# Optimization experiments

Measured on AMD Instinct MI355X. Metric: run time of the kernel, lower is better.

The kernel has to match this reference:

```python
import jax, jax.numpy as jnp
import numpy as np

N = 16384   # nodes
E = 262144  # edges (avg degree 16)
H = 256     # hidden_dim
R = 32      # num_radial


def _lin(k, fi, fo):
    return jax.random.normal(k, (fi, fo), jnp.float32) / np.float32(np.sqrt(fi))


def setup_inputs() -> dict:
    key = jax.random.key(0)
    ks = jax.random.split(key, 16)
    h = jax.random.normal(ks[0], (N, H), jnp.float32)
    pos = jax.random.normal(ks[1], (N, 3), jnp.float32)
    edge_index = jax.random.randint(ks[2], (2, E), 0, N, dtype=jnp.int32)
    return {
        'h': h, 'pos': pos,
        # radial_basis: Linear(1,R), SiLU, Linear(R,R)
        'rb_w1': _lin(ks[3], 1, R), 'rb_b1': jnp.zeros((R,), jnp.float32),
        'rb_w2': _lin(ks[4], R, R), 'rb_b2': jnp.zeros((R,), jnp.float32),
        # edge_network: Linear(2H+R,H), SiLU, Linear(H,H), LayerNorm(H)
        'en_w1': _lin(ks[5], 2 * H + R, H), 'en_b1': jnp.zeros((H,), jnp.float32),
        'en_w2': _lin(ks[6], H, H), 'en_b2': jnp.zeros((H,), jnp.float32),
        'en_g': jnp.ones((H,), jnp.float32), 'en_bt': jnp.zeros((H,), jnp.float32),
        # node_network: Linear(2H,H), SiLU, Linear(H,H), LayerNorm(H)
        'nn_w1': _lin(ks[7], 2 * H, H), 'nn_b1': jnp.zeros((H,), jnp.float32),
        'nn_w2': _lin(ks[8], H, H), 'nn_b2': jnp.zeros((H,), jnp.float32),
        'nn_g': jnp.ones((H,), jnp.float32), 'nn_bt': jnp.zeros((H,), jnp.float32),
        # coord_network: Linear(H,H//2), SiLU, Linear(H//2,1), Tanh
        'cn_w1': _lin(ks[9], H, H // 2), 'cn_b1': jnp.zeros((H // 2,), jnp.float32),
        'cn_w2': _lin(ks[10], H // 2, 1), 'cn_b2': jnp.zeros((1,), jnp.float32),
        'edge_index': edge_index,
    }


def _ln(x, g, b, eps=1e-5):
    mu = jnp.mean(x, axis=-1, keepdims=True)
    var = jnp.var(x, axis=-1, keepdims=True)
    return (x - mu) / jnp.sqrt(var + eps) * g + b


def reference(h, pos, rb_w1, rb_b1, rb_w2, rb_b2,
              en_w1, en_b1, en_w2, en_b2, en_g, en_bt,
              nn_w1, nn_b1, nn_w2, nn_b2, nn_g, nn_bt,
              cn_w1, cn_b1, cn_w2, cn_b2, edge_index):
    row, col = edge_index[0], edge_index[1]
    rel_pos = pos[col] - pos[row]                                   # [E,3]
    # torch: norm(rel_pos + 1e-8) -> scalar eps added to the vector first
    dist = jnp.linalg.norm(rel_pos + 1e-8, axis=-1, keepdims=True)  # [E,1]
    radial = jax.nn.silu(dist @ rb_w1 + rb_b1) @ rb_w2 + rb_b2      # [E,R]
    edge_feat = jnp.concatenate([h[row], h[col], radial], axis=-1)  # [E,2H+R]
    edge_msg = _ln(jax.nn.silu(edge_feat @ en_w1 + en_b1) @ en_w2 + en_b2,
                   en_g, en_bt)                                     # [E,H]
    # PyG propagate with aggr='add': sum messages at target nodes (col)
    node_msg = jax.ops.segment_sum(edge_msg, col, num_segments=h.shape[0])
    hn_in = jnp.concatenate([h, node_msg], axis=-1)                 # [N,2H]
    h_updated = _ln(jax.nn.silu(hn_in @ nn_w1 + nn_b1) @ nn_w2 + nn_b2,
                    nn_g, nn_bt)                                    # [N,H]
    coord_w = jnp.tanh(jax.nn.silu(edge_msg @ cn_w1 + cn_b1) @ cn_w2 + cn_b2)  # [E,1]
    weighted = rel_pos * coord_w                                    # [E,3]
    pos_updates = jnp.zeros_like(pos).at[row].add(-weighted).at[col].add(weighted)
    return h_updated, pos_updates
```

## Files before the change

### kernel.cpp

```cpp
#include <hip/hip_runtime.h>
#include <hip/hip_bf16.h>


#define NN 16384
#define EE 262144
#define HH 256
#define RR 32

typedef __bf16 bf16x8 __attribute__((ext_vector_type(8)));
typedef float f32x4 __attribute__((ext_vector_type(4)));

typedef const void __attribute__((address_space(1)))* gas_ptr;
typedef void __attribute__((address_space(3)))* las_ptr;

__device__ __forceinline__ void gload16(const void* g, void* l) {
  __builtin_amdgcn_global_load_lds((gas_ptr)g, (las_ptr)l, 16, 0, 0);
}

__device__ __forceinline__ float silu_f(float x) { return x / (1.0f + __expf(-x)); }

__device__ __forceinline__ unsigned short bf_bits(float x) {
  union { __hip_bfloat16 b; unsigned short u; } v;
  v.b = __float2bfloat16(x);
  return v.u;
}
__device__ __forceinline__ float ubf(unsigned short u) {
  return __uint_as_float(((unsigned)u) << 16);
}

__global__ __launch_bounds__(256) void conv_h_kernel(const float* __restrict__ src,
                                                     __hip_bfloat16* __restrict__ dst,
                                                     int n4) {
  int i = blockIdx.x * 256 + threadIdx.x;
  if (i >= n4) return;
  float4 v = ((const float4*)src)[i];
  __hip_bfloat16* d = dst + (size_t)i * 4;
  d[0] = __float2bfloat16(v.x);
  d[1] = __float2bfloat16(v.y);
  d[2] = __float2bfloat16(v.z);
  d[3] = __float2bfloat16(v.w);
}

__global__ __launch_bounds__(256) void prep_w_kernel(
    const float* __restrict__ en_w1, const float* __restrict__ en_w2,
    const float* __restrict__ nn_w1, const float* __restrict__ nn_w2,
    const float* __restrict__ cn_w1, const float* __restrict__ rb_w2,
    const float* __restrict__ rb_b2, const float* __restrict__ en_b1,
    __hip_bfloat16* __restrict__ W2T, __hip_bfloat16* __restrict__ NW1T,
    __hip_bfloat16* __restrict__ NW2T, __hip_bfloat16* __restrict__ CW1T,
    __hip_bfloat16* __restrict__ W1abT, __hip_bfloat16* __restrict__ RWT,
    float* __restrict__ b1p) {
  int bid = blockIdx.x, tid = threadIdx.x;
  if (bid < 256) {
    int i = bid * 256 + tid, k = i >> 8, c = i & 255;
    W2T[(size_t)c * 256 + k] = __float2bfloat16(en_w2[i]);
  } else if (bid < 768) {
    int i = (bid - 256) * 256 + tid, k = i >> 8, c = i & 255;
    NW1T[(size_t)c * 512 + k] = __float2bfloat16(nn_w1[i]);
  } else if (bid < 1024) {
    int i = (bid - 768) * 256 + tid, k = i >> 8, c = i & 255;
    NW2T[(size_t)c * 256 + k] = __float2bfloat16(nn_w2[i]);
  } else if (bid < 1152) {
    int i = (bid - 1024) * 256 + tid, k = i >> 7, c = i & 127;
    CW1T[(size_t)c * 256 + k] = __float2bfloat16(cn_w1[i]);
  } else if (bid < 1408) {
    int i = (bid - 1152) * 256 + tid, k = i >> 8, c = i & 255;
    W1abT[(size_t)c * 256 + k] = __float2bfloat16(en_w1[i]);
  } else if (bid < 1664) {
    int i = (bid - 1408) * 256 + tid, k = i >> 8, c = i & 255;
    W1abT[(size_t)(256 + c) * 256 + k] = __float2bfloat16(en_w1[256 * 256 + i]);
  } else if (bid < 1696) {
    int t = (bid - 1664) * 256 + tid;
    int c = t >> 5, i = t & 31;
    float s = 0.f;
#pragma unroll
    for (int j = 0; j < 32; ++j) s += rb_w2[i * 32 + j] * en_w1[(512 + j) * 256 + c];
    RWT[c * 32 + i] = __float2bfloat16(s);
  } else {
    int c = tid;
    float s = en_b1[c];
#pragma unroll
    for (int j = 0; j < 32; ++j) s += rb_b2[j] * en_w1[(512 + j) * 256 + c];
    b1p[c] = s;
  }
}

__global__ __launch_bounds__(256) void count_kernel(const int* __restrict__ ei,
                                                    int* __restrict__ counts) {
  int e = blockIdx.x * 256 + threadIdx.x;
  if (e >= EE) return;
  atomicAdd(&counts[ei[EE + e]], 1);
}

__global__ __launch_bounds__(256) void scanA_kernel(const int* __restrict__ counts,
                                                    int* __restrict__ bsum) {
  __shared__ int ws[4];
  int t = threadIdx.x;
  int v = counts[blockIdx.x * 256 + t];
#pragma unroll
  for (int m = 1; m < 64; m <<= 1) v += __shfl_xor(v, m, 64);
  if ((t & 63) == 0) ws[t >> 6] = v;
  __syncthreads();
  if (t == 0) bsum[blockIdx.x] = ws[0] + ws[1] + ws[2] + ws[3];
}

__global__ __launch_bounds__(64) void scanB_kernel(const int* __restrict__ bsum,
                                                   int* __restrict__ bbase,
                                                   int* __restrict__ offs) {
  int t = threadIdx.x;
  int v = bsum[t], x = v;
#pragma unroll
  for (int d = 1; d < 64; d <<= 1) {
    int y = __shfl_up(x, d, 64);
    if (t >= d) x += y;
  }
  bbase[t] = x - v;
  if (t == 63) offs[NN] = x;
}

__global__ __launch_bounds__(256) void scanC_kernel(const int* __restrict__ counts,
                                                    const int* __restrict__ bbase,
                                                    int* __restrict__ offs,
                                                    int* __restrict__ cursor) {
  __shared__ int wtot[4];
  int t = threadIdx.x, wv = t >> 6, ln = t & 63;
  int base = blockIdx.x * 256;
  int v = counts[base + t], x = v;
#pragma unroll
  for (int d = 1; d < 64; d <<= 1) {
    int y = __shfl_up(x, d, 64);
    if (ln >= d) x += y;
  }
  if (ln == 63) wtot[wv] = x;
  __syncthreads();
  int add = bbase[blockIdx.x];
  for (int k = 0; k < wv; ++k) add += wtot[k];
  int excl = add + x - v;
  offs[base + t] = excl;
  cursor[base + t] = excl;
}

__global__ __launch_bounds__(256) void scatter_kernel(const int* __restrict__ ei,
                                                      int* __restrict__ cursor,
                                                      int* __restrict__ elist) {
  int e = blockIdx.x * 256 + threadIdx.x;
  if (e >= EE) return;
  int c = ei[EE + e];
  int p = atomicAdd(&cursor[c], 1);
  elist[p] = e;
}

__global__ __launch_bounds__(512) void pgemm_kernel(const __hip_bfloat16* __restrict__ A,
                                                    const __hip_bfloat16* __restrict__ BT,
                                                    __hip_bfloat16* __restrict__ out) {
  const int tid = threadIdx.x, w = tid >> 6, l = tid & 63, r = l & 15, g = l >> 4;
  const int n0 = blockIdx.x * 64;
  f32x4 acc[4][4];
#pragma unroll
  for (int a = 0; a < 4; ++a)
#pragma unroll
    for (int b = 0; b < 4; ++b) acc[a][b] = (f32x4){0.f, 0.f, 0.f, 0.f};
  for (int ks = 0; ks < 8; ++ks) {
    bf16x8 af[4], bfr[4];
#pragma unroll
    for (int fm = 0; fm < 4; ++fm)
      af[fm] = *(const bf16x8*)(A + (size_t)(n0 + fm * 16 + r) * 256 + ks * 32 + g * 8);
#pragma unroll
    for (int fn = 0; fn < 4; ++fn)
      bfr[fn] = *(const bf16x8*)(BT + (size_t)(w * 64 + fn * 16 + r) * 256 + ks * 32 + g * 8);
#pragma unroll
    for (int fm = 0; fm < 4; ++fm)
#pragma unroll
      for (int fn = 0; fn < 4; ++fn)
        acc[fm][fn] =
            __builtin_amdgcn_mfma_f32_16x16x32_bf16(af[fm], bfr[fn], acc[fm][fn], 0, 0, 0);
  }
#pragma unroll
  for (int fm = 0; fm < 4; ++fm)
#pragma unroll
    for (int fn = 0; fn < 4; ++fn) {
      int col = w * 64 + fn * 16 + r;
#pragma unroll
      for (int q = 0; q < 4; ++q) {
        int row = n0 + fm * 16 + g * 4 + q;
        out[(size_t)row * 512 + col] = __float2bfloat16(acc[fm][fn][q]);
      }
    }
}

__global__ __launch_bounds__(256, 4) void hidden_kernel(
    const __hip_bfloat16* __restrict__ Pb, const int* __restrict__ ei,
    const float* __restrict__ pos, const float* __restrict__ rb_w1,
    const float* __restrict__ rb_b1, const __hip_bfloat16* __restrict__ RWT,
    const float* __restrict__ b1p, const int* __restrict__ elist,
    __hip_bfloat16* __restrict__ hiddenb) {
  const int tid = threadIdx.x, w = tid >> 6, l = tid & 63, r = l & 15, g = l >> 4;
  const int slot = blockIdx.x * 64 + w * 16 + r;
  int e = elist[slot];
  int nr = ei[e], nc = ei[EE + e];
  float dx = pos[nc * 3 + 0] - pos[nr * 3 + 0] + 1e-8f;
  float dy = pos[nc * 3 + 1] - pos[nr * 3 + 1] + 1e-8f;
  float dz = pos[nc * 3 + 2] - pos[nr * 3 + 2] + 1e-8f;
  float d = sqrtf(dx * dx + dy * dy + dz * dz);
  bf16x8 sfrag;
#pragma unroll
  for (int j = 0; j < 8; ++j) {
    float x = d * rb_w1[g * 8 + j] + rb_b1[g * 8 + j];
    sfrag[j] = (__bf16)silu_f(x);
  }
  const unsigned short* Pu = (const unsigned short*)Pb;
  unsigned short* H = (unsigned short*)hiddenb;
  const size_t rowbase = (size_t)slot * 256;
  const int swz = (slot & 7) << 3;
#pragma unroll 4
  for (int t = 0; t < 16; ++t) {
    bf16x8 afr = *(const bf16x8*)(RWT + (size_t)(t * 16 + r) * 32 + g * 8);
    f32x4 rad = __builtin_amdgcn_mfma_f32_16x16x32_bf16(
        afr, sfrag, (f32x4){0.f, 0.f, 0.f, 0.f}, 0, 0, 0);
    int cbase = t * 16 + g * 4;
    ushort4 p1 = *(const ushort4*)(Pu + (size_t)nr * 512 + cbase);
    ushort4 p2 = *(const ushort4*)(Pu + (size_t)nc * 512 + 256 + cbase);
    float4 b1v = *(const float4*)(b1p + cbase);
    ushort4 o;
    o.x = bf_bits(silu_f(rad[0] + ubf(p1.x) + ubf(p2.x) + b1v.x));
    o.y = bf_bits(silu_f(rad[1] + ubf(p1.y) + ubf(p2.y) + b1v.y));
    o.z = bf_bits(silu_f(rad[2] + ubf(p1.z) + ubf(p2.z) + b1v.z));
    o.w = bf_bits(silu_f(rad[3] + ubf(p1.w) + ubf(p2.w) + b1v.w));
    *(ushort4*)(H + rowbase + (cbase ^ swz)) = o;
  }
}

__global__ __launch_bounds__(512, 4) void msg_kernel(
    const __hip_bfloat16* __restrict__ hiddenb, const int* __restrict__ ei,
    const float* __restrict__ pos, const __hip_bfloat16* __restrict__ W2T,
    const float* __restrict__ en_b2, const float* __restrict__ en_g,
    const float* __restrict__ en_bt, const __hip_bfloat16* __restrict__ CW1T,
    const float* __restrict__ cn_b1, const float* __restrict__ cn_w2,
    const float* __restrict__ cn_b2, const int* __restrict__ elist,
    float* __restrict__ nmsg, float* __restrict__ pos_out) {
  __shared__ __align__(16) __hip_bfloat16 A2[64 * 256];
  __shared__ float relb[64][3];
  __shared__ int srow[64], scol[64];
  __shared__ float red[8][64], redsq[8][64];
  __shared__ float mv[64][2];

  const int tid = threadIdx.x, w = tid >> 6, l = tid & 63, r = l & 15, g = l >> 4;
  const int e0 = blockIdx.x * 64;
  unsigned short* A2u = (unsigned short*)A2;

#pragma unroll
  for (int pass = 0; pass < 4; ++pass)
    gload16((const char*)hiddenb + (size_t)e0 * 512 + pass * 8192 + w * 1024 + l * 16,
            (char*)A2 + pass * 8192 + w * 1024);

  if (tid < 64) {
    int e = elist[e0 + tid];
    int r2 = ei[e], c2 = ei[EE + e];
    srow[tid] = r2;
    scol[tid] = c2;
    relb[tid][0] = pos[c2 * 3 + 0] - pos[r2 * 3 + 0];
    relb[tid][1] = pos[c2 * 3 + 1] - pos[r2 * 3 + 1];
    relb[tid][2] = pos[c2 * 3 + 2] - pos[r2 * 3 + 2];
  }
  __syncthreads();

  f32x4 acc[2][4];
#pragma unroll
  for (int a = 0; a < 2; ++a)
#pragma unroll
    for (int b = 0; b < 4; ++b) acc[a][b] = (f32x4){0.f, 0.f, 0.f, 0.f};
  for (int ks = 0; ks < 8; ++ks) {
    bf16x8 af[2], bfr[4];
#pragma unroll
    for (int mf = 0; mf < 2; ++mf)
      af[mf] = *(const bf16x8*)(W2T + (size_t)(w * 32 + mf * 16 + r) * 256 + ks * 32 + g * 8);
#pragma unroll
    for (int nf = 0; nf < 4; ++nf) {
      int row = nf * 16 + r;
      bfr[nf] = *(const bf16x8*)(A2 + row * 256 + ((ks * 32 + g * 8) ^ ((row & 7) << 3)));
    }
#pragma unroll
    for (int mf = 0; mf < 2; ++mf)
#pragma unroll
      for (int nf = 0; nf < 4; ++nf)
        acc[mf][nf] =
            __builtin_amdgcn_mfma_f32_16x16x32_bf16(af[mf], bfr[nf], acc[mf][nf], 0, 0, 0);
  }
  {
    float4 b2v0 = *(const float4*)(en_b2 + w * 32 + g * 4);
    float4 b2v1 = *(const float4*)(en_b2 + w * 32 + 16 + g * 4);
#pragma unroll
    for (int nf = 0; nf < 4; ++nf) {
      acc[0][nf][0] += b2v0.x;
      acc[0][nf][1] += b2v0.y;
      acc[0][nf][2] += b2v0.z;
      acc[0][nf][3] += b2v0.w;
      acc[1][nf][0] += b2v1.x;
      acc[1][nf][1] += b2v1.y;
      acc[1][nf][2] += b2v1.z;
      acc[1][nf][3] += b2v1.w;
    }
  }

#pragma unroll
  for (int nf = 0; nf < 4; ++nf) {
    float s = 0.f, sq = 0.f;
#pragma unroll
    for (int mf = 0; mf < 2; ++mf)
#pragma unroll
      for (int q = 0; q < 4; ++q) {
        float v = acc[mf][nf][q];
        s += v;
        sq += v * v;
      }
    s += __shfl_xor(s, 16, 64);
    s += __shfl_xor(s, 32, 64);
    sq += __shfl_xor(sq, 16, 64);
    sq += __shfl_xor(sq, 32, 64);
    if (l < 16) {
      red[w][nf * 16 + l] = s;
      redsq[w][nf * 16 + l] = sq;
    }
  }
  __syncthreads();
  if (tid < 64) {
    float s = 0.f, sq = 0.f;
#pragma unroll
    for (int k = 0; k < 8; ++k) {
      s += red[k][tid];
      sq += redsq[k][tid];
    }
    float mean = s * (1.0f / HH);
    float var = sq * (1.0f / HH) - mean * mean;
    mv[tid][0] = mean;
    mv[tid][1] = rsqrtf(var + 1e-5f);
  }
  __syncthreads();

  {
    float4 gv0 = *(const float4*)(en_g + w * 32 + g * 4);
    float4 gv1 = *(const float4*)(en_g + w * 32 + 16 + g * 4);
    float4 bv0 = *(const float4*)(en_bt + w * 32 + g * 4);
    float4 bv1 = *(const float4*)(en_bt + w * 32 + 16 + g * 4);
#pragma unroll
    for (int nf = 0; nf < 4; ++nf) {
      int e = nf * 16 + r;
      float mm = mv[e][0], rs = mv[e][1];
      int sz = (e & 7) << 3;
      ushort4 o0, o1;
      o0.x = bf_bits((acc[0][nf][0] - mm) * rs * gv0.x + bv0.x);
      o0.y = bf_bits((acc[0][nf][1] - mm) * rs * gv0.y + bv0.y);
      o0.z = bf_bits((acc[0][nf][2] - mm) * rs * gv0.z + bv0.z);
      o0.w = bf_bits((acc[0][nf][3] - mm) * rs * gv0.w + bv0.w);
      o1.x = bf_bits((acc[1][nf][0] - mm) * rs * gv1.x + bv1.x);
      o1.y = bf_bits((acc[1][nf][1] - mm) * rs * gv1.y + bv1.y);
      o1.z = bf_bits((acc[1][nf][2] - mm) * rs * gv1.z + bv1.z);
      o1.w = bf_bits((acc[1][nf][3] - mm) * rs * gv1.w + bv1.w);
      *(ushort4*)(A2u + (size_t)e * 256 + ((w * 32 + g * 4) ^ sz)) = o0;
      *(ushort4*)(A2u + (size_t)e * 256 + ((w * 32 + 16 + g * 4) ^ sz)) = o1;
    }
  }
  __syncthreads();

  f32x4 cacc[4];
#pragma unroll
  for (int a = 0; a < 4; ++a) cacc[a] = (f32x4){0.f, 0.f, 0.f, 0.f};
  for (int ks = 0; ks < 8; ++ks) {
    bf16x8 af = *(const bf16x8*)(CW1T + (size_t)(w * 16 + r) * 256 + ks * 32 + g * 8);
    bf16x8 bfr[4];
#pragma unroll
    for (int nf = 0; nf < 4; ++nf) {
      int row = nf * 16 + r;
      bfr[nf] = *(const bf16x8*)(A2 + row * 256 + ((ks * 32 + g * 8) ^ ((row & 7) << 3)));
    }
#pragma unroll
    for (int nf = 0; nf < 4; ++nf)
      cacc[nf] = __builtin_amdgcn_mfma_f32_16x16x32_bf16(af, bfr[nf], cacc[nf], 0, 0, 0);
  }
  {
    float4 cb1v = *(const float4*)(cn_b1 + w * 16 + g * 4);
    float4 cw2v = *(const float4*)(cn_w2 + w * 16 + g * 4);
#pragma unroll
    for (int nf = 0; nf < 4; ++nf) {
      float v = silu_f(cacc[nf][0] + cb1v.x) * cw2v.x +
                silu_f(cacc[nf][1] + cb1v.y) * cw2v.y +
                silu_f(cacc[nf][2] + cb1v.z) * cw2v.z +
                silu_f(cacc[nf][3] + cb1v.w) * cw2v.w;
      v += __shfl_xor(v, 16, 64);
      v += __shfl_xor(v, 32, 64);
      if (l < 16) red[w][nf * 16 + l] = v;
    }
  }

  {
    int c = tid & 255, half = tid >> 8;
    int rbeg = half * 32, rend = rbeg + 32;
    float run = 0.f;
    int cur = scol[rbeg];
    for (int row = rbeg; row < rend; ++row) {
      int nd = scol[row];
      if (nd != cur) {
        atomicAdd(&nmsg[(size_t)cur * 256 + c], run);
        run = 0.f;
        cur = nd;
      }
      run += ubf(A2u[(size_t)row * 256 + (c ^ ((row & 7) << 3))]);
    }
    atomicAdd(&nmsg[(size_t)cur * 256 + c], run);
  }
  __syncthreads();
  if (tid < 64) {
    float s = cn_b2[0];
#pragma unroll
    for (int k = 0; k < 8; ++k) s += red[k][tid];
    float wgt = tanhf(s);
    float ax = relb[tid][0], ay = relb[tid][1], az = relb[tid][2];
    int rr = srow[tid], cc = scol[tid];
    atomicAdd(&pos_out[rr * 3 + 0], -wgt * ax);
    atomicAdd(&pos_out[rr * 3 + 1], -wgt * ay);
    atomicAdd(&pos_out[rr * 3 + 2], -wgt * az);
    atomicAdd(&pos_out[cc * 3 + 0], wgt * ax);
    atomicAdd(&pos_out[cc * 3 + 1], wgt * ay);
    atomicAdd(&pos_out[cc * 3 + 2], wgt * az);
  }
}

__global__ __launch_bounds__(512, 4) void node_kernel(
    const __hip_bfloat16* __restrict__ hb, const float* __restrict__ nmsg,
    const __hip_bfloat16* __restrict__ NW1T, const float* __restrict__ nn_b1,
    const __hip_bfloat16* __restrict__ NW2T, const float* __restrict__ nn_b2,
    const float* __restrict__ nn_g, const float* __restrict__ nn_bt,
    float* __restrict__ out_h) {
  __shared__ __align__(16) __hip_bfloat16 A2[32 * 264];
  __shared__ float red[8][32], redsq[8][32];
  __shared__ float mv[32][2];
  __shared__ float gb[HH], btb[HH];
  const int tid = threadIdx.x, w = tid >> 6, l = tid & 63, r = l & 15, g = l >> 4;
  const int n0 = blockIdx.x * 32;
  if (tid < 256) {
    gb[tid] = nn_g[tid];
    btb[tid] = nn_bt[tid];
  }

  f32x4 acc[2][2];
#pragma unroll
  for (int a = 0; a < 2; ++a)
#pragma unroll
    for (int b = 0; b < 2; ++b) acc[a][b] = (f32x4){0.f, 0.f, 0.f, 0.f};
  for (int ks = 0; ks < 8; ++ks) {
    bf16x8 af[2], bfr[2];
#pragma unroll
    for (int fm = 0; fm < 2; ++fm)
      af[fm] = *(const bf16x8*)(hb + (size_t)(n0 + fm * 16 + r) * 256 + ks * 32 + g * 8);
#pragma unroll
    for (int fn = 0; fn < 2; ++fn)
      bfr[fn] = *(const bf16x8*)(NW1T + (size_t)(w * 32 + fn * 16 + r) * 512 + ks * 32 + g * 8);
#pragma unroll
    for (int fm = 0; fm < 2; ++fm)
#pragma unroll
      for (int fn = 0; fn < 2; ++fn)
        acc[fm][fn] =
            __builtin_amdgcn_mfma_f32_16x16x32_bf16(af[fm], bfr[fn], acc[fm][fn], 0, 0, 0);
  }
  for (int ks = 0; ks < 8; ++ks) {
    bf16x8 af[2], bfr[2];
#pragma unroll
    for (int fm = 0; fm < 2; ++fm) {
      const float* src = nmsg + (size_t)(n0 + fm * 16 + r) * 256 + ks * 32 + g * 8;
      float4 a0 = *(const float4*)src;
      float4 a1 = *(const float4*)(src + 4);
      bf16x8 v;
      v[0] = (__bf16)a0.x;
      v[1] = (__bf16)a0.y;
      v[2] = (__bf16)a0.z;
      v[3] = (__bf16)a0.w;
      v[4] = (__bf16)a1.x;
      v[5] = (__bf16)a1.y;
      v[6] = (__bf16)a1.z;
      v[7] = (__bf16)a1.w;
      af[fm] = v;
    }
#pragma unroll
    for (int fn = 0; fn < 2; ++fn)
      bfr[fn] =
          *(const bf16x8*)(NW1T + (size_t)(w * 32 + fn * 16 + r) * 512 + 256 + ks * 32 + g * 8);
#pragma unroll
    for (int fm = 0; fm < 2; ++fm)
#pragma unroll
      for (int fn = 0; fn < 2; ++fn)
        acc[fm][fn] =
            __builtin_amdgcn_mfma_f32_16x16x32_bf16(af[fm], bfr[fn], acc[fm][fn], 0, 0, 0);
  }
  __syncthreads();
#pragma unroll
  for (int fn = 0; fn < 2; ++fn) {
    int col = w * 32 + fn * 16 + r;
    float b1 = nn_b1[col];
#pragma unroll
    for (int fm = 0; fm < 2; ++fm)
#pragma unroll
      for (int q = 0; q < 4; ++q) {
        int row = fm * 16 + g * 4 + q;
        A2[row * 264 + col] = __float2bfloat16(silu_f(acc[fm][fn][q] + b1));
      }
  }
  __syncthreads();

#pragma unroll
  for (int a = 0; a < 2; ++a)
#pragma unroll
    for (int b = 0; b < 2; ++b) acc[a][b] = (f32x4){0.f, 0.f, 0.f, 0.f};
  for (int ks = 0; ks < 8; ++ks) {
    bf16x8 af[2], bfr[2];
#pragma unroll
    for (int fm = 0; fm < 2; ++fm)
      af[fm] = *(const bf16x8*)(A2 + (fm * 16 + r) * 264 + ks * 32 + g * 8);
#pragma unroll
    for (int fn = 0; fn < 2; ++fn)
      bfr[fn] = *(const bf16x8*)(NW2T + (size_t)(w * 32 + fn * 16 + r) * 256 + ks * 32 + g * 8);
#pragma unroll
    for (int fm = 0; fm < 2; ++fm)
#pragma unroll
      for (int fn = 0; fn < 2; ++fn)
        acc[fm][fn] =
            __builtin_amdgcn_mfma_f32_16x16x32_bf16(af[fm], bfr[fn], acc[fm][fn], 0, 0, 0);
  }
#pragma unroll
  for (int fn = 0; fn < 2; ++fn) {
    float b2 = nn_b2[w * 32 + fn * 16 + r];
#pragma unroll
    for (int fm = 0; fm < 2; ++fm)
#pragma unroll
      for (int q = 0; q < 4; ++q) acc[fm][fn][q] += b2;
  }
#pragma unroll
  for (int fm = 0; fm < 2; ++fm)
#pragma unroll
    for (int q = 0; q < 4; ++q) {
      float s = acc[fm][0][q] + acc[fm][1][q];
      float sq = acc[fm][0][q] * acc[fm][0][q] + acc[fm][1][q] * acc[fm][1][q];
#pragma unroll
      for (int m = 1; m < 16; m <<= 1) {
        s += __shfl_xor(s, m, 64);
        sq += __shfl_xor(sq, m, 64);
      }
      if (r == 0) {
        red[w][fm * 16 + g * 4 + q] = s;
        redsq[w][fm * 16 + g * 4 + q] = sq;
      }
    }
  __syncthreads();
  if (tid < 32) {
    float s = 0.f, sq = 0.f;
#pragma unroll
    for (int k = 0; k < 8; ++k) {
      s += red[k][tid];
      sq += redsq[k][tid];
    }
    float mean = s * (1.0f / HH);
    float var = sq * (1.0f / HH) - mean * mean;
    mv[tid][0] = mean;
    mv[tid][1] = rsqrtf(var + 1e-5f);
  }
  __syncthreads();
#pragma unroll
  for (int fn = 0; fn < 2; ++fn) {
    int col = w * 32 + fn * 16 + r;
    float gg = gb[col], bb = btb[col];
#pragma unroll
    for (int fm = 0; fm < 2; ++fm)
#pragma unroll
      for (int q = 0; q < 4; ++q) {
        int row = fm * 16 + g * 4 + q;
        out_h[(size_t)(n0 + row) * HH + col] =
            (acc[fm][fn][q] - mv[row][0]) * mv[row][1] * gg + bb;
      }
  }
}

extern "C" void kernel_launch(void* const* d_in, const int* in_sizes, int n_in,
                              void* d_out, int out_size, void* d_ws, size_t ws_size,
                              hipStream_t stream) {
  const float* h = (const float*)d_in[0];
  const float* pos = (const float*)d_in[1];
  const float* rb_w1 = (const float*)d_in[2];
  const float* rb_b1 = (const float*)d_in[3];
  const float* rb_w2 = (const float*)d_in[4];
  const float* rb_b2 = (const float*)d_in[5];
  const float* en_w1 = (const float*)d_in[6];
  const float* en_b1 = (const float*)d_in[7];
  const float* en_w2 = (const float*)d_in[8];
  const float* en_b2 = (const float*)d_in[9];
  const float* en_g = (const float*)d_in[10];
  const float* en_bt = (const float*)d_in[11];
  const float* nn_w1 = (const float*)d_in[12];
  const float* nn_b1 = (const float*)d_in[13];
  const float* nn_w2 = (const float*)d_in[14];
  const float* nn_b2 = (const float*)d_in[15];
  const float* nn_g = (const float*)d_in[16];
  const float* nn_bt = (const float*)d_in[17];
  const float* cn_w1 = (const float*)d_in[18];
  const float* cn_b1 = (const float*)d_in[19];
  const float* cn_w2 = (const float*)d_in[20];
  const float* cn_b2 = (const float*)d_in[21];
  const int* ei = (const int*)d_in[22];

  float* out_h = (float*)d_out;
  float* out_pos = out_h + (size_t)NN * HH;

  char* p = (char*)d_ws;
  auto alloc = [&p](size_t bytes) {
    char* q = p;
    p += (bytes + 255) & ~(size_t)255;
    return q;
  };
  __hip_bfloat16* hb = (__hip_bfloat16*)alloc((size_t)NN * HH * 2);
  __hip_bfloat16* Pb = (__hip_bfloat16*)alloc((size_t)NN * 512 * 2);
  __hip_bfloat16* W1abT = (__hip_bfloat16*)alloc((size_t)512 * 256 * 2);
  __hip_bfloat16* W2T = (__hip_bfloat16*)alloc((size_t)256 * 256 * 2);
  __hip_bfloat16* NW1T = (__hip_bfloat16*)alloc((size_t)256 * 512 * 2);
  __hip_bfloat16* NW2T = (__hip_bfloat16*)alloc((size_t)256 * 256 * 2);
  __hip_bfloat16* CW1T = (__hip_bfloat16*)alloc((size_t)128 * 256 * 2);
  __hip_bfloat16* RWT = (__hip_bfloat16*)alloc((size_t)256 * 32 * 2);
  float* b1p = (float*)alloc((size_t)256 * 4);
  __hip_bfloat16* hiddenb = (__hip_bfloat16*)alloc((size_t)EE * HH * 2);
  float* nmsg = (float*)alloc((size_t)NN * HH * 4);
  int* counts = (int*)alloc((size_t)NN * 4);
  int* offs = (int*)alloc((size_t)(NN + 1) * 4);
  int* cursor = (int*)alloc((size_t)NN * 4);
  int* elist = (int*)alloc((size_t)EE * 4);
  int* bsum = (int*)alloc((size_t)64 * 4);
  int* bbase = (int*)alloc((size_t)64 * 4);

  hipMemsetAsync(out_pos, 0, (size_t)NN * 3 * sizeof(float), stream);
  hipMemsetAsync(counts, 0, (size_t)NN * sizeof(int), stream);
  hipMemsetAsync(nmsg, 0, (size_t)NN * HH * sizeof(float), stream);

  prep_w_kernel<<<1697, 256, 0, stream>>>(en_w1, en_w2, nn_w1, nn_w2, cn_w1, rb_w2, rb_b2,
                                          en_b1, W2T, NW1T, NW2T, CW1T, W1abT, RWT, b1p);
  conv_h_kernel<<<(NN * HH / 4 + 255) / 256, 256, 0, stream>>>(h, hb, NN * HH / 4);
  count_kernel<<<EE / 256, 256, 0, stream>>>(ei, counts);
  scanA_kernel<<<NN / 256, 256, 0, stream>>>(counts, bsum);
  scanB_kernel<<<1, 64, 0, stream>>>(bsum, bbase, offs);
  scanC_kernel<<<NN / 256, 256, 0, stream>>>(counts, bbase, offs, cursor);
  scatter_kernel<<<EE / 256, 256, 0, stream>>>(ei, cursor, elist);
  pgemm_kernel<<<NN / 64, 512, 0, stream>>>(hb, W1abT, Pb);
  hidden_kernel<<<EE / 64, 256, 0, stream>>>(Pb, ei, pos, rb_w1, rb_b1, RWT, b1p, elist,
                                             hiddenb);
  msg_kernel<<<EE / 64, 512, 0, stream>>>(hiddenb, ei, pos, W2T, en_b2, en_g, en_bt, CW1T,
                                          cn_b1, cn_w2, cn_b2, elist, nmsg, out_pos);
  node_kernel<<<NN / 32, 512, 0, stream>>>(hb, nmsg, NW1T, nn_b1, NW2T, nn_b2, nn_g, nn_bt,
                                           out_h);
}
```

Baseline: 540.8 us.

## Fuse hidden and message kernels into one per-wave edge kernel

```diff
diff --git a/kernel.cpp b/kernel.cpp
--- a/kernel.cpp
+++ b/kernel.cpp
@@ -9,13 +9,6 @@
 
 typedef __bf16 bf16x8 __attribute__((ext_vector_type(8)));
 typedef float f32x4 __attribute__((ext_vector_type(4)));
-
-typedef const void __attribute__((address_space(1)))* gas_ptr;
-typedef void __attribute__((address_space(3)))* las_ptr;
-
-__device__ __forceinline__ void gload16(const void* g, void* l) {
-  __builtin_amdgcn_global_load_lds((gas_ptr)g, (las_ptr)l, 16, 0, 0);
-}
 
 __device__ __forceinline__ float silu_f(float x) { return x / (1.0f + __expf(-x)); }
 
@@ -188,30 +181,40 @@
     }
 }
 
-__global__ __launch_bounds__(256, 4) void hidden_kernel(
+#define WROW 260
+__global__ __launch_bounds__(256, 3) void edge_fused_kernel(
     const __hip_bfloat16* __restrict__ Pb, const int* __restrict__ ei,
     const float* __restrict__ pos, const float* __restrict__ rb_w1,
     const float* __restrict__ rb_b1, const __hip_bfloat16* __restrict__ RWT,
-    const float* __restrict__ b1p, const int* __restrict__ elist,
-    __hip_bfloat16* __restrict__ hiddenb) {
+    const float* __restrict__ b1p, const __hip_bfloat16* __restrict__ W2T,
+    const float* __restrict__ en_b2, const float* __restrict__ en_g,
+    const float* __restrict__ en_bt, const __hip_bfloat16* __restrict__ CW1T,
+    const float* __restrict__ cn_b1, const float* __restrict__ cn_w2,
+    const float* __restrict__ cn_b2, const int* __restrict__ elist,
+    float* __restrict__ nmsg, float* __restrict__ pos_out) {
+  __shared__ __align__(16) unsigned short ldsbuf[4][16 * WROW];
+  __shared__ int colmeta[4][16];
   const int tid = threadIdx.x, w = tid >> 6, l = tid & 63, r = l & 15, g = l >> 4;
+  unsigned short* WB = &ldsbuf[w][0];
+
   const int slot = blockIdx.x * 64 + w * 16 + r;
-  int e = elist[slot];
-  int nr = ei[e], nc = ei[EE + e];
-  float dx = pos[nc * 3 + 0] - pos[nr * 3 + 0] + 1e-8f;
-  float dy = pos[nc * 3 + 1] - pos[nr * 3 + 1] + 1e-8f;
-  float dz = pos[nc * 3 + 2] - pos[nr * 3 + 2] + 1e-8f;
-  float d = sqrtf(dx * dx + dy * dy + dz * dz);
+  const int e = elist[slot];
+  const int nr = ei[e], nc = ei[EE + e];
+  float dx = pos[nc * 3 + 0] - pos[nr * 3 + 0];
+  float dy = pos[nc * 3 + 1] - pos[nr * 3 + 1];
+  float dz = pos[nc * 3 + 2] - pos[nr * 3 + 2];
+  float ex = dx + 1e-8f, ey = dy + 1e-8f, ez = dz + 1e-8f;
+  float d = sqrtf(ex * ex + ey * ey + ez * ez);
+  if (g == 0) colmeta[w][r] = nc;
+
   bf16x8 sfrag;
 #pragma unroll
   for (int j = 0; j < 8; ++j) {
     float x = d * rb_w1[g * 8 + j] + rb_b1[g * 8 + j];
     sfrag[j] = (__bf16)silu_f(x);
   }
+
   const unsigned short* Pu = (const unsigned short*)Pb;
-  unsigned short* H = (unsigned short*)hiddenb;
-  const size_t rowbase = (size_t)slot * 256;
-  const int swz = (slot & 7) << 3;
 #pragma unroll 4
   for (int t = 0; t < 16; ++t) {
     bf16x8 afr = *(const bf16x8*)(RWT + (size_t)(t * 16 + r) * 32 + g * 8);
@@ -226,202 +229,109 @@
     o.y = bf_bits(silu_f(rad[1] + ubf(p1.y) + ubf(p2.y) + b1v.y));
     o.z = bf_bits(silu_f(rad[2] + ubf(p1.z) + ubf(p2.z) + b1v.z));
     o.w = bf_bits(silu_f(rad[3] + ubf(p1.w) + ubf(p2.w) + b1v.w));
-    *(ushort4*)(H + rowbase + (cbase ^ swz)) = o;
-  }
-}
-
-__global__ __launch_bounds__(512, 4) void msg_kernel(
-    const __hip_bfloat16* __restrict__ hiddenb, const int* __restrict__ ei,
-    const float* __restrict__ pos, const __hip_bfloat16* __restrict__ W2T,
-    const float* __restrict__ en_b2, const float* __restrict__ en_g,
-    const float* __restrict__ en_bt, const __hip_bfloat16* __restrict__ CW1T,
-    const float* __restrict__ cn_b1, const float* __restrict__ cn_w2,
-    const float* __restrict__ cn_b2, const int* __restrict__ elist,
-    float* __restrict__ nmsg, float* __restrict__ pos_out) {
-  __shared__ __align__(16) __hip_bfloat16 A2[64 * 256];
-  __shared__ float relb[64][3];
-  __shared__ int srow[64], scol[64];
-  __shared__ float red[8][64], redsq[8][64];
-  __shared__ float mv[64][2];
-
-  const int tid = threadIdx.x, w = tid >> 6, l = tid & 63, r = l & 15, g = l >> 4;
-  const int e0 = blockIdx.x * 64;
-  unsigned short* A2u = (unsigned short*)A2;
-
-#pragma unroll
-  for (int pass = 0; pass < 4; ++pass)
-    gload16((const char*)hiddenb + (size_t)e0 * 512 + pass * 8192 + w * 1024 + l * 16,
-            (char*)A2 + pass * 8192 + w * 1024);
-
-  if (tid < 64) {
-    int e = elist[e0 + tid];
-    int r2 = ei[e], c2 = ei[EE + e];
-    srow[tid] = r2;
-    scol[tid] = c2;
-    relb[tid][0] = pos[c2 * 3 + 0] - pos[r2 * 3 + 0];
-    relb[tid][1] = pos[c2 * 3 + 1] - pos[r2 * 3 + 1];
-    relb[tid][2] = pos[c2 * 3 + 2] - pos[r2 * 3 + 2];
-  }
-  __syncthreads();
-
-  f32x4 acc[2][4];
-#pragma unroll
-  for (int a = 0; a < 2; ++a)
-#pragma unroll
-    for (int b = 0; b < 4; ++b) acc[a][b] = (f32x4){0.f, 0.f, 0.f, 0.f};
+    *(ushort4*)(WB + r * WROW + cbase) = o;
+  }
+
+  f32x4 acc[16];
+#pragma unroll
+  for (int a = 0; a < 16; ++a) acc[a] = (f32x4){0.f, 0.f, 0.f, 0.f};
   for (int ks = 0; ks < 8; ++ks) {
-    bf16x8 af[2], bfr[4];
-#pragma unroll
-    for (int mf = 0; mf < 2; ++mf)
-      af[mf] = *(const bf16x8*)(W2T + (size_t)(w * 32 + mf * 16 + r) * 256 + ks * 32 + g * 8);
-#pragma unroll
-    for (int nf = 0; nf < 4; ++nf) {
-      int row = nf * 16 + r;
-      bfr[nf] = *(const bf16x8*)(A2 + row * 256 + ((ks * 32 + g * 8) ^ ((row & 7) << 3)));
-    }
-#pragma unroll
-    for (int mf = 0; mf < 2; ++mf)
-#pragma unroll
-      for (int nf = 0; nf < 4; ++nf)
-        acc[mf][nf] =
-            __builtin_amdgcn_mfma_f32_16x16x32_bf16(af[mf], bfr[nf], acc[mf][nf], 0, 0, 0);
-  }
+    bf16x8 bfr = *(const bf16x8*)(WB + r * WROW + ks * 32 + g * 8);
+#pragma unroll
+    for (int mf = 0; mf < 16; ++mf) {
+      bf16x8 af = *(const bf16x8*)(W2T + (size_t)(mf * 16 + r) * 256 + ks * 32 + g * 8);
+      acc[mf] = __builtin_amdgcn_mfma_f32_16x16x32_bf16(af, bfr, acc[mf], 0, 0, 0);
+    }
+  }
+
+  float s = 0.f, sq = 0.f;
+#pragma unroll
+  for (int mf = 0; mf < 16; ++mf) {
+    float4 b2v = *(const float4*)(en_b2 + mf * 16 + g * 4);
+#pragma unroll
+    for (int q = 0; q < 4; ++q) {
+      float v = acc[mf][q] + ((const float*)&b2v)[q];
+      acc[mf][q] = v;
+      s += v;
+      sq += v * v;
+    }
+  }
+  s += __shfl_xor(s, 16, 64);
+  s += __shfl_xor(s, 32, 64);
+  sq += __shfl_xor(sq, 16, 64);
+  sq += __shfl_xor(sq, 32, 64);
+  float mean = s * (1.0f / HH);
+  float rstd = rsqrtf(sq * (1.0f / HH) - mean * mean + 1e-5f);
+
+#pragma unroll
+  for (int mf = 0; mf < 16; ++mf) {
+    float4 gv = *(const float4*)(en_g + mf * 16 + g * 4);
+    float4 bv = *(const float4*)(en_bt + mf * 16 + g * 4);
+    ushort4 o;
+    o.x = bf_bits((acc[mf][0] - mean) * rstd * gv.x + bv.x);
+    o.y = bf_bits((acc[mf][1] - mean) * rstd * gv.y + bv.y);
+    o.z = bf_bits((acc[mf][2] - mean) * rstd * gv.z + bv.z);
+    o.w = bf_bits((acc[mf][3] - mean) * rstd * gv.w + bv.w);
+    *(ushort4*)(WB + r * WROW + mf * 16 + g * 4) = o;
+  }
+
+  f32x4 cacc[8];
+#pragma unroll
+  for (int a = 0; a < 8; ++a) cacc[a] = (f32x4){0.f, 0.f, 0.f, 0.f};
+  for (int ks = 0; ks < 8; ++ks) {
+    bf16x8 bfr = *(const bf16x8*)(WB + r * WROW + ks * 32 + g * 8);
+#pragma unroll
+    for (int mf = 0; mf < 8; ++mf) {
+      bf16x8 af = *(const bf16x8*)(CW1T + (size_t)(mf * 16 + r) * 256 + ks * 32 + g * 8);
+      cacc[mf] = __builtin_amdgcn_mfma_f32_16x16x32_bf16(af, bfr, cacc[mf], 0, 0, 0);
+    }
+  }
+  float vsum = 0.f;
+#pragma unroll
+  for (int mf = 0; mf < 8; ++mf) {
+    float4 cb = *(const float4*)(cn_b1 + mf * 16 + g * 4);
+    float4 cw = *(const float4*)(cn_w2 + mf * 16 + g * 4);
+    vsum += silu_f(cacc[mf][0] + cb.x) * cw.x;
+    vsum += silu_f(cacc[mf][1] + cb.y) * cw.y;
+    vsum += silu_f(cacc[mf][2] + cb.z) * cw.z;
+    vsum += silu_f(cacc[mf][3] + cb.w) * cw.w;
+  }
+  vsum += __shfl_xor(vsum, 16, 64);
+  vsum += __shfl_xor(vsum, 32, 64);
+  if (g == 0) {
+    float wgt = tanhf(vsum + cn_b2[0]);
+    atomicAdd(&pos_out[nr * 3 + 0], -wgt * dx);
+    atomicAdd(&pos_out[nr * 3 + 1], -wgt * dy);
+    atomicAdd(&pos_out[nr * 3 + 2], -wgt * dz);
+    atomicAdd(&pos_out[nc * 3 + 0], wgt * dx);
+    atomicAdd(&pos_out[nc * 3 + 1], wgt * dy);
+    atomicAdd(&pos_out[nc * 3 + 2], wgt * dz);
+  }
+
   {
-    float4 b2v0 = *(const float4*)(en_b2 + w * 32 + g * 4);
-    float4 b2v1 = *(const float4*)(en_b2 + w * 32 + 16 + g * 4);
-#pragma unroll
-    for (int nf = 0; nf < 4; ++nf) {
-      acc[0][nf][0] += b2v0.x;
-      acc[0][nf][1] += b2v0.y;
-      acc[0][nf][2] += b2v0.z;
-      acc[0][nf][3] += b2v0.w;
-      acc[1][nf][0] += b2v1.x;
-      acc[1][nf][1] += b2v1.y;
-      acc[1][nf][2] += b2v1.z;
-      acc[1][nf][3] += b2v1.w;
-    }
-  }
-
-#pragma unroll
-  for (int nf = 0; nf < 4; ++nf) {
-    float s = 0.f, sq = 0.f;
-#pragma unroll
-    for (int mf = 0; mf < 2; ++mf)
-#pragma unroll
-      for (int q = 0; q < 4; ++q) {
-        float v = acc[mf][nf][q];
-        s += v;
-        sq += v * v;
-      }
-    s += __shfl_xor(s, 16, 64);
-    s += __shfl_xor(s, 32, 64);
-    sq += __shfl_xor(sq, 16, 64);
-    sq += __shfl_xor(sq, 32, 64);
-    if (l < 16) {
-      red[w][nf * 16 + l] = s;
-      redsq[w][nf * 16 + l] = sq;
-    }
-  }
-  __syncthreads();
-  if (tid < 64) {
-    float s = 0.f, sq = 0.f;
-#pragma unroll
-    for (int k = 0; k < 8; ++k) {
-      s += red[k][tid];
-      sq += redsq[k][tid];
-    }
-    float mean = s * (1.0f / HH);
-    float var = sq * (1.0f / HH) - mean * mean;
-    mv[tid][0] = mean;
-    mv[tid][1] = rsqrtf(var + 1e-5f);
-  }
-  __syncthreads();
-
-  {
-    float4 gv0 = *(const float4*)(en_g + w * 32 + g * 4);
-    float4 gv1 = *(const float4*)(en_g + w * 32 + 16 + g * 4);
-    float4 bv0 = *(const float4*)(en_bt + w * 32 + g * 4);
-    float4 bv1 = *(const float4*)(en_bt + w * 32 + 16 + g * 4);
-#pragma unroll
-    for (int nf = 0; nf < 4; ++nf) {
-      int e = nf * 16 + r;
-      float mm = mv[e][0], rs = mv[e][1];
-      int sz = (e & 7) << 3;
-      ushort4 o0, o1;
-      o0.x = bf_bits((acc[0][nf][0] - mm) * rs * gv0.x + bv0.x);
-      o0.y = bf_bits((acc[0][nf][1] - mm) * rs * gv0.y + bv0.y);
-      o0.z = bf_bits((acc[0][nf][2] - mm) * rs * gv0.z + bv0.z);
-      o0.w = bf_bits((acc[0][nf][3] - mm) * rs * gv0.w + bv0.w);
-      o1.x = bf_bits((acc[1][nf][0] - mm) * rs * gv1.x + bv1.x);
-      o1.y = bf_bits((acc[1][nf][1] - mm) * rs * gv1.y + bv1.y);
-      o1.z = bf_bits((acc[1][nf][2] - mm) * rs * gv1.z + bv1.z);
-      o1.w = bf_bits((acc[1][nf][3] - mm) * rs * gv1.w + bv1.w);
-      *(ushort4*)(A2u + (size_t)e * 256 + ((w * 32 + g * 4) ^ sz)) = o0;
-      *(ushort4*)(A2u + (size_t)e * 256 + ((w * 32 + 16 + g * 4) ^ sz)) = o1;
-    }
-  }
-  __syncthreads();
-
-  f32x4 cacc[4];
-#pragma unroll
-  for (int a = 0; a < 4; ++a) cacc[a] = (f32x4){0.f, 0.f, 0.f, 0.f};
-  for (int ks = 0; ks < 8; ++ks) {
-    bf16x8 af = *(const bf16x8*)(CW1T + (size_t)(w * 16 + r) * 256 + ks * 32 + g * 8);
-    bf16x8 bfr[4];
-#pragma unroll
-    for (int nf = 0; nf < 4; ++nf) {
-      int row = nf * 16 + r;
-      bfr[nf] = *(const bf16x8*)(A2 + row * 256 + ((ks * 32 + g * 8) ^ ((row & 7) << 3)));
-    }
-#pragma unroll
-    for (int nf = 0; nf < 4; ++nf)
-      cacc[nf] = __builtin_amdgcn_mfma_f32_16x16x32_bf16(af, bfr[nf], cacc[nf], 0, 0, 0);
-  }
-  {
-    float4 cb1v = *(const float4*)(cn_b1 + w * 16 + g * 4);
-    float4 cw2v = *(const float4*)(cn_w2 + w * 16 + g * 4);
-#pragma unroll
-    for (int nf = 0; nf < 4; ++nf) {
-      float v = silu_f(cacc[nf][0] + cb1v.x) * cw2v.x +
-                silu_f(cacc[nf][1] + cb1v.y) * cw2v.y +
-                silu_f(cacc[nf][2] + cb1v.z) * cw2v.z +
-                silu_f(cacc[nf][3] + cb1v.w) * cw2v.w;
-      v += __shfl_xor(v, 16, 64);
-      v += __shfl_xor(v, 32, 64);
-      if (l < 16) red[w][nf * 16 + l] = v;
-    }
-  }
-
-  {
-    int c = tid & 255, half = tid >> 8;
-    int rbeg = half * 32, rend = rbeg + 32;
-    float run = 0.f;
-    int cur = scol[rbeg];
-    for (int row = rbeg; row < rend; ++row) {
-      int nd = scol[row];
+    float run0 = 0.f, run1 = 0.f, run2 = 0.f, run3 = 0.f;
+    int cur = colmeta[w][0];
+#pragma unroll 4
+    for (int row = 0; row < 16; ++row) {
+      int nd = colmeta[w][row];
       if (nd != cur) {
-        atomicAdd(&nmsg[(size_t)cur * 256 + c], run);
-        run = 0.f;
+        atomicAdd(&nmsg[(size_t)cur * 256 + l * 4 + 0], run0);
+        atomicAdd(&nmsg[(size_t)cur * 256 + l * 4 + 1], run1);
+        atomicAdd(&nmsg[(size_t)cur * 256 + l * 4 + 2], run2);
+        atomicAdd(&nmsg[(size_t)cur * 256 + l * 4 + 3], run3);
+        run0 = run1 = run2 = run3 = 0.f;
         cur = nd;
       }
-      run += ubf(A2u[(size_t)row * 256 + (c ^ ((row & 7) << 3))]);
-    }
-    atomicAdd(&nmsg[(size_t)cur * 256 + c], run);
-  }
-  __syncthreads();
-  if (tid < 64) {
-    float s = cn_b2[0];
-#pragma unroll
-    for (int k = 0; k < 8; ++k) s += red[k][tid];
-    float wgt = tanhf(s);
-    float ax = relb[tid][0], ay = relb[tid][1], az = relb[tid][2];
-    int rr = srow[tid], cc = scol[tid];
-    atomicAdd(&pos_out[rr * 3 + 0], -wgt * ax);
-    atomicAdd(&pos_out[rr * 3 + 1], -wgt * ay);
-    atomicAdd(&pos_out[rr * 3 + 2], -wgt * az);
-    atomicAdd(&pos_out[cc * 3 + 0], wgt * ax);
-    atomicAdd(&pos_out[cc * 3 + 1], wgt * ay);
-    atomicAdd(&pos_out[cc * 3 + 2], wgt * az);
+      ushort4 mv4 = *(const ushort4*)(WB + row * WROW + l * 4);
+      run0 += ubf(mv4.x);
+      run1 += ubf(mv4.y);
+      run2 += ubf(mv4.z);
+      run3 += ubf(mv4.w);
+    }
+    atomicAdd(&nmsg[(size_t)cur * 256 + l * 4 + 0], run0);
+    atomicAdd(&nmsg[(size_t)cur * 256 + l * 4 + 1], run1);
+    atomicAdd(&nmsg[(size_t)cur * 256 + l * 4 + 2], run2);
+    atomicAdd(&nmsg[(size_t)cur * 256 + l * 4 + 3], run3);
   }
 }
 
@@ -623,7 +533,6 @@
   __hip_bfloat16* CW1T = (__hip_bfloat16*)alloc((size_t)128 * 256 * 2);
   __hip_bfloat16* RWT = (__hip_bfloat16*)alloc((size_t)256 * 32 * 2);
   float* b1p = (float*)alloc((size_t)256 * 4);
-  __hip_bfloat16* hiddenb = (__hip_bfloat16*)alloc((size_t)EE * HH * 2);
   float* nmsg = (float*)alloc((size_t)NN * HH * 4);
   int* counts = (int*)alloc((size_t)NN * 4);
   int* offs = (int*)alloc((size_t)(NN + 1) * 4);
@@ -645,10 +554,9 @@
   scanC_kernel<<<NN / 256, 256, 0, stream>>>(counts, bbase, offs, cursor);
   scatter_kernel<<<EE / 256, 256, 0, stream>>>(ei, cursor, elist);
   pgemm_kernel<<<NN / 64, 512, 0, stream>>>(hb, W1abT, Pb);
-  hidden_kernel<<<EE / 64, 256, 0, stream>>>(Pb, ei, pos, rb_w1, rb_b1, RWT, b1p, elist,
-                                             hiddenb);
-  msg_kernel<<<EE / 64, 512, 0, stream>>>(hiddenb, ei, pos, W2T, en_b2, en_g, en_bt, CW1T,
-                                          cn_b1, cn_w2, cn_b2, elist, nmsg, out_pos);
+  edge_fused_kernel<<<EE / 64, 256, 0, stream>>>(Pb, ei, pos, rb_w1, rb_b1, RWT, b1p, W2T,
+                                                 en_b2, en_g, en_bt, CW1T, cn_b1, cn_w2,
+                                                 cn_b2, elist, nmsg, out_pos);
   node_kernel<<<NN / 32, 512, 0, stream>>>(hb, nmsg, NW1T, nn_b1, NW2T, nn_b2, nn_g, nn_bt,
                                            out_h);
 }
```

Measured after the change: 773.7 us. +43.1%, slower.
